# Performance work log

Measured on AMD Instinct MI355X. Metric: run time of the kernel, lower is better.

The kernel has to match this reference:

```python
import jax, jax.numpy as jnp
import numpy as np

N = 100000   # nodes
E = 800000   # edges
H = 64       # hidden_channels (also input feature dim via lazy Linear)
OUT = 2      # out_channels
G = 64       # graphs in batch
EPS = 1e-5   # BatchNorm eps
N_PRE, N_CONV, N_POST = 3, 6, 3


def setup_inputs() -> dict:
    key = jax.random.key(0)
    ks = jax.random.split(key, 20)
    s = 0.1
    inp = {
        "x": jax.random.normal(ks[0], (N, H), jnp.float32),
        "edge_index": jax.random.randint(ks[1], (2, E), 0, N, dtype=jnp.int64),
        "batch": jnp.sort(jax.random.randint(ks[2], (N,), 0, G, dtype=jnp.int64)),
        # pre-processing MLP + BN params
        "pre_W": jax.random.normal(ks[3], (N_PRE, H, H), jnp.float32) * s,
        "pre_b": jax.random.normal(ks[4], (N_PRE, H), jnp.float32) * s,
        "pre_g": jnp.ones((N_PRE, H), jnp.float32),
        "pre_beta": jnp.zeros((N_PRE, H), jnp.float32),
        # GCNConv params (weight + bias per layer)
        "conv_W": jax.random.normal(ks[5], (N_CONV, H, H), jnp.float32) * s,
        "conv_b": jax.random.normal(ks[6], (N_CONV, H), jnp.float32) * s,
        # post-processing MLP + BN params
        "post_W": jax.random.normal(ks[7], (N_POST, H, H), jnp.float32) * s,
        "post_b": jax.random.normal(ks[8], (N_POST, H), jnp.float32) * s,
        "post_g": jnp.ones((N_POST, H), jnp.float32),
        "post_beta": jnp.zeros((N_POST, H), jnp.float32),
        # final head: H->H, H->H, H->OUT
        "fin_W0": jax.random.normal(ks[9], (H, H), jnp.float32) * s,
        "fin_b0": jax.random.normal(ks[10], (H,), jnp.float32) * s,
        "fin_W1": jax.random.normal(ks[11], (H, H), jnp.float32) * s,
        "fin_b1": jax.random.normal(ks[12], (H,), jnp.float32) * s,
        "fin_W2": jax.random.normal(ks[13], (H, OUT), jnp.float32) * s,
        "fin_b2": jax.random.normal(ks[14], (OUT,), jnp.float32) * s,
    }
    return inp


def _bn(h, g, b):
    # BatchNorm1d, training mode: biased batch statistics over node dim
    m = h.mean(0)
    v = h.var(0)
    return (h - m) * jax.lax.rsqrt(v + EPS) * g + b


def _gcn(h, src, dst, dinv, W, b):
    # PyG GCNConv: h' = D^-1/2 (A+I) D^-1/2 (h W) + b, sum-aggregated at dst
    hw = h @ W                                   # [N,H]
    norm = dinv[src] * dinv[dst]                 # [E]
    agg = jax.ops.segment_sum(hw[src] * norm[:, None], dst, num_segments=N)
    agg = agg + hw * (dinv * dinv)[:, None]      # self-loop contribution
    return agg + b


def reference(x, edge_index, batch, pre_W, pre_b, pre_g, pre_beta,
              conv_W, conv_b, post_W, post_b, post_g, post_beta,
              fin_W0, fin_b0, fin_W1, fin_b1, fin_W2, fin_b2):
    src, dst = edge_index[0], edge_index[1]
    # gcn_norm degree with self-loops (in-degree at dst), edge_weight = 1
    deg = jax.ops.segment_sum(jnp.ones((E,), x.dtype), dst, num_segments=N) + 1.0
    dinv = jax.lax.rsqrt(deg)

    h = x
    # pre-processing: Linear -> BN, relu except last
    for i in range(N_PRE):
        h = _bn(h @ pre_W[i] + pre_b[i], pre_g[i], pre_beta[i])
        if i != N_PRE - 1:
            h = jax.nn.relu(h)
    # GCNConv stack with residual adds
    for i in range(N_CONV):
        h = _gcn(h, src, dst, dinv, conv_W[i], conv_b[i]) + h
        if i != N_CONV - 1:
            h = jax.nn.relu(h)
    # post-processing: Linear -> BN, relu except last
    for i in range(N_POST):
        h = _bn(h @ post_W[i] + post_b[i], post_g[i], post_beta[i])
        if i != N_POST - 1:
            h = jax.nn.relu(h)
    # global_mean_pool over graphs
    counts = jax.ops.segment_sum(jnp.ones((N,), h.dtype), batch, num_segments=G)
    pooled = jax.ops.segment_sum(h, batch, num_segments=G) / jnp.maximum(counts, 1.0)[:, None]
    # final head (dropout is identity in eval)
    z = jax.nn.relu(pooled @ fin_W0 + fin_b0)
    z = jax.nn.relu(z @ fin_W1 + fin_b1)
    return z @ fin_W2 + fin_b2
```

## Files before the change

### kernel.cpp

```cpp
#include <hip/hip_runtime.h>

#define N_NODES 100000
#define N_EDGES 800000
#define HID 64
#define NGRAPH 64
#define OUTC 2
#define BN_EPS 1e-5f
#define GEMM_BLK ((N_NODES + 63) / 64)
#define POOL_SUB 16
#define BSHIFT 11
#define NBUCK 64
#define NBUCK_ACT ((N_NODES + (1 << BSHIFT) - 1) >> BSHIFT)
#define NEB_BLK ((N_EDGES + 2047) / 2048)

typedef __attribute__((ext_vector_type(8))) short bf16x8;
typedef __attribute__((ext_vector_type(4))) float f32x4;
typedef __attribute__((ext_vector_type(2))) float f32x2;

__device__ __forceinline__ unsigned short f2bf(float f) {
    unsigned int u = __float_as_uint(f);
    u = (u + 0x7FFFu + ((u >> 16) & 1u)) >> 16;
    return (unsigned short)u;
}
__device__ __forceinline__ float bflo(unsigned int u) { return __uint_as_float(u << 16); }
__device__ __forceinline__ float bfhi(unsigned int u) { return __uint_as_float(u & 0xFFFF0000u); }
__device__ __forceinline__ unsigned int bfpack(float a, float b) {
    return (unsigned int)f2bf(a) | ((unsigned int)f2bf(b) << 16);
}
__device__ __forceinline__ f32x2 bfpair(unsigned int w) {
    f32x2 p;
    p.x = __uint_as_float(w << 16);
    p.y = __uint_as_float(w & 0xFFFF0000u);
    return p;
}
__device__ __forceinline__ f32x2 pk_add(f32x2 a, f32x2 b) {
    f32x2 d;
    asm("v_pk_add_f32 %0, %1, %2" : "=v"(d) : "v"(a), "v"(b));
    return d;
}

template <int IN_MODE, bool IN_FP32, bool ADD_BIAS, bool ROW_SCALE, bool STATS>
__global__ __launch_bounds__(256) void k_gemm(const void* __restrict__ Xv,
                                              const float* __restrict__ W,
                                              const float* __restrict__ bias,
                                              const float* __restrict__ dinv,
                                              const float* __restrict__ scsh,
                                              unsigned short* __restrict__ Y,
                                              float* __restrict__ partial, int n) {
    __shared__ __align__(16) unsigned short sXb[64][72];
    __shared__ __align__(16) unsigned short sWT[64][72];
    __shared__ float sDinv[64];
    const int tid  = threadIdx.x;
    const int row0 = blockIdx.x * 64;

    #pragma unroll
    for (int i = tid; i < 1024; i += 256) {
        int k = i >> 4, c4 = (i & 15) << 2;
        float4 w = *reinterpret_cast<const float4*>(&W[k * 64 + c4]);
        sWT[c4 + 0][k] = f2bf(w.x);
        sWT[c4 + 1][k] = f2bf(w.y);
        sWT[c4 + 2][k] = f2bf(w.z);
        sWT[c4 + 3][k] = f2bf(w.w);
    }
    if (IN_FP32) {
        const float* X = (const float*)Xv;
        #pragma unroll
        for (int f = tid; f < 1024; f += 256) {
            int r = f >> 4, c4 = (f & 15) << 2;
            float4 v = make_float4(0.f, 0.f, 0.f, 0.f);
            if (row0 + r < n)
                v = *reinterpret_cast<const float4*>(&X[(size_t)(row0 + r) * HID + c4]);
            if (IN_MODE >= 1) {
                float4 sc = *reinterpret_cast<const float4*>(&scsh[c4]);
                float4 sh = *reinterpret_cast<const float4*>(&scsh[64 + c4]);
                v.x = v.x * sc.x + sh.x; v.y = v.y * sc.y + sh.y;
                v.z = v.z * sc.z + sh.z; v.w = v.w * sc.w + sh.w;
                if (IN_MODE == 2) {
                    v.x = fmaxf(v.x, 0.f); v.y = fmaxf(v.y, 0.f);
                    v.z = fmaxf(v.z, 0.f); v.w = fmaxf(v.w, 0.f);
                }
            }
            sXb[r][c4 + 0] = f2bf(v.x);
            sXb[r][c4 + 1] = f2bf(v.y);
            sXb[r][c4 + 2] = f2bf(v.z);
            sXb[r][c4 + 3] = f2bf(v.w);
        }
    } else {
        const unsigned short* X = (const unsigned short*)Xv;
        #pragma unroll
        for (int f = tid; f < 512; f += 256) {
            int r = f >> 3, c8 = (f & 7) << 3;
            uint4 u = make_uint4(0u, 0u, 0u, 0u);
            if (row0 + r < n)
                u = *reinterpret_cast<const uint4*>(&X[(size_t)(row0 + r) * HID + c8]);
            if (IN_MODE >= 1) {
                float v[8];
                v[0] = bflo(u.x); v[1] = bfhi(u.x);
                v[2] = bflo(u.y); v[3] = bfhi(u.y);
                v[4] = bflo(u.z); v[5] = bfhi(u.z);
                v[6] = bflo(u.w); v[7] = bfhi(u.w);
                #pragma unroll
                for (int k = 0; k < 8; ++k) {
                    v[k] = v[k] * scsh[c8 + k] + scsh[64 + c8 + k];
                    if (IN_MODE == 2) v[k] = fmaxf(v[k], 0.f);
                }
                u.x = bfpack(v[0], v[1]); u.y = bfpack(v[2], v[3]);
                u.z = bfpack(v[4], v[5]); u.w = bfpack(v[6], v[7]);
            }
            *reinterpret_cast<uint4*>(&sXb[r][c8]) = u;
        }
    }
    if (ROW_SCALE && tid < 64)
        sDinv[tid] = (row0 + tid < n) ? dinv[row0 + tid] : 0.f;
    __syncthreads();

    const int lane = tid & 63;
    const int wv   = tid >> 6;
    const int cl   = lane & 15;
    const int kg   = lane >> 4;
    const int col  = (wv << 4) + cl;

    const f32x4 zero = {0.f, 0.f, 0.f, 0.f};
    f32x4 acc[4];
    #pragma unroll
    for (int m = 0; m < 4; ++m) acc[m] = zero;

    #pragma unroll
    for (int k0 = 0; k0 < 64; k0 += 32) {
        bf16x8 bfrag = *reinterpret_cast<const bf16x8*>(&sWT[col][k0 + (kg << 3)]);
        #pragma unroll
        for (int m = 0; m < 4; ++m) {
            bf16x8 afrag = *reinterpret_cast<const bf16x8*>(&sXb[(m << 4) + cl][k0 + (kg << 3)]);
            acc[m] = __builtin_amdgcn_mfma_f32_16x16x32_bf16(afrag, bfrag, acc[m], 0, 0, 0);
        }
    }

    const float bb = ADD_BIAS ? bias[col] : 0.f;
    float colS = 0.f, colQ = 0.f;
    #pragma unroll
    for (int m = 0; m < 4; ++m) {
        #pragma unroll
        for (int j = 0; j < 4; ++j) {
            int rl = (m << 4) + (kg << 2) + j;
            int r  = row0 + rl;
            if (r < n) {
                float s = ROW_SCALE ? sDinv[rl] : 1.f;
                float o = acc[m][j] * s + bb;
                Y[(size_t)r * HID + col] = f2bf(o);
                if (STATS) { colS += o; colQ += o * o; }
            }
        }
    }
    if (STATS) {
        colS += __shfl_xor(colS, 16); colQ += __shfl_xor(colQ, 16);
        colS += __shfl_xor(colS, 32); colQ += __shfl_xor(colQ, 32);
        if (kg == 0) {
            partial[blockIdx.x * 128 + col]      = colS;
            partial[blockIdx.x * 128 + 64 + col] = colQ;
        }
    }
}

__global__ __launch_bounds__(256) void k_statsfin(const float* __restrict__ partial,
                                                  const float* __restrict__ g,
                                                  const float* __restrict__ beta,
                                                  float* __restrict__ scsh, int n) {
    int c = blockIdx.x, t = threadIdx.x;
    float S = 0.f, Q = 0.f;
    for (int b = t; b < GEMM_BLK; b += 256) {
        S += partial[b * 128 + c];
        Q += partial[b * 128 + 64 + c];
    }
    __shared__ float ss[256], sq[256];
    ss[t] = S; sq[t] = Q;
    __syncthreads();
    for (int off = 128; off > 0; off >>= 1) {
        if (t < off) { ss[t] += ss[t + off]; sq[t] += sq[t + off]; }
        __syncthreads();
    }
    if (t == 0) {
        float nf = (float)n;
        float m  = ss[0] / nf;
        float v  = sq[0] / nf - m * m;
        float sc = rsqrtf(v + BN_EPS) * g[c];
        scsh[c]      = sc;
        scsh[64 + c] = beta[c] - m * sc;
    }
}

__global__ __launch_bounds__(256) void k_hist(const int* __restrict__ dst,
                                              int* __restrict__ histmat) {
    __shared__ int lh[NBUCK];
    int t = threadIdx.x;
    if (t < NBUCK) lh[t] = 0;
    __syncthreads();
    int base = blockIdx.x * 2048;
    for (int i = t; i < 2048; i += 256) {
        int e = base + i;
        if (e < N_EDGES) atomicAdd(&lh[dst[e] >> BSHIFT], 1);
    }
    __syncthreads();
    if (t < NBUCK) histmat[blockIdx.x * NBUCK + t] = lh[t];
}

__global__ __launch_bounds__(256) void k_escan(const int* __restrict__ histmat,
                                               int* __restrict__ blockoff,
                                               int* __restrict__ bucketbase) {
    __shared__ int csum[4][NBUCK];
    __shared__ int cbase[4][NBUCK];
    __shared__ int tot[NBUCK + 1];
    int t = threadIdx.x;
    int b = t & 63, c = t >> 6;
    const int CHUNK = (NEB_BLK + 3) / 4;
    int lo = c * CHUNK, hi = min(lo + CHUNK, NEB_BLK);
    int s = 0;
    #pragma unroll 8
    for (int blk = lo; blk < hi; ++blk) s += histmat[blk * NBUCK + b];
    csum[c][b] = s;
    __syncthreads();
    if (t < NBUCK) {
        int r = 0;
        #pragma unroll
        for (int c2 = 0; c2 < 4; ++c2) { cbase[c2][t] = r; r += csum[c2][t]; }
        tot[t] = r;
    }
    __syncthreads();
    if (t == 0) {
        int r = 0;
        for (int b2 = 0; b2 < NBUCK; ++b2) { int v = tot[b2]; tot[b2] = r; r += v; }
        tot[NBUCK] = r;
    }
    __syncthreads();
    if (t <= NBUCK) bucketbase[t] = tot[t];
    int r = cbase[c][b];
    #pragma unroll 8
    for (int blk = lo; blk < hi; ++blk) {
        blockoff[blk * NBUCK + b] = r;
        r += histmat[blk * NBUCK + b];
    }
}

__global__ __launch_bounds__(256) void k_reorder(const int* __restrict__ src,
                                                 const int* __restrict__ dst,
                                                 const int* __restrict__ blockoff,
                                                 const int* __restrict__ bucketbase,
                                                 int2* __restrict__ esort) {
    __shared__ int lcur[NBUCK];
    int t = threadIdx.x;
    if (t < NBUCK) lcur[t] = 0;
    __syncthreads();
    int base = blockIdx.x * 2048;
    for (int i = t; i < 2048; i += 256) {
        int e = base + i;
        if (e < N_EDGES) {
            int d = dst[e];
            int b = d >> BSHIFT;
            int r = atomicAdd(&lcur[b], 1);
            esort[bucketbase[b] + blockoff[blockIdx.x * NBUCK + b] + r] =
                make_int2(src[e], d);
        }
    }
}

__global__ __launch_bounds__(256) void k_csr(const int2* __restrict__ esort,
                                             const int* __restrict__ bucketbase,
                                             int* __restrict__ rowptr,
                                             int* __restrict__ colidx,
                                             float* __restrict__ dinv) {
    __shared__ int lh[1 << BSHIFT];
    __shared__ int ctot[256];
    int t = threadIdx.x;
    int b = blockIdx.x;
    int node0 = b << BSHIFT;
    int nNodes = min(1 << BSHIFT, N_NODES - node0);
    int e0 = bucketbase[b], e1 = bucketbase[b + 1];
    #pragma unroll
    for (int i = t; i < (1 << BSHIFT); i += 256) lh[i] = 0;
    __syncthreads();
    for (int e = e0 + t; e < e1; e += 256)
        atomicAdd(&lh[esort[e].y - node0], 1);
    __syncthreads();
    int c0 = t * 8;
    int cnt[8];
    int s = 0;
    #pragma unroll
    for (int j = 0; j < 8; ++j) { cnt[j] = lh[c0 + j]; s += cnt[j]; }
    ctot[t] = s;
    __syncthreads();
    int v = ctot[t];
    for (int off = 1; off < 256; off <<= 1) {
        int x = (t >= off) ? ctot[t - off] : 0;
        __syncthreads();
        ctot[t] += x;
        __syncthreads();
    }
    int run = ctot[t] - v;
    #pragma unroll
    for (int j = 0; j < 8; ++j) {
        int idx = c0 + j;
        int cv = cnt[j];
        lh[idx] = run;
        if (idx < nNodes) {
            rowptr[node0 + idx] = e0 + run;
            dinv[node0 + idx]   = rsqrtf((float)cv + 1.f);
        }
        run += cv;
    }
    __syncthreads();
    for (int e = e0 + t; e < e1; e += 256) {
        int2 ed = esort[e];
        int r = atomicAdd(&lh[ed.y - node0], 1);
        colidx[e0 + r] = ed.x;
    }
    if (b == 0 && t == 0) rowptr[N_NODES] = N_EDGES;
}

template <int IN_MODE, bool RELU>
__global__ __launch_bounds__(256) void k_gather(const int* __restrict__ rowptr,
                                                const int* __restrict__ colidx,
                                                const unsigned short* __restrict__ HWb,
                                                const unsigned short* __restrict__ Hin,
                                                const float* __restrict__ dinv,
                                                const float* __restrict__ bias,
                                                const float* __restrict__ scsh,
                                                unsigned short* __restrict__ Out) {
    __shared__ float red[4][8][64];
    const int wv   = threadIdx.x >> 6;
    const int d    = blockIdx.x * 4 + wv;
    const int lane = threadIdx.x & 63;
    const int slot = lane >> 3;
    const int c8   = (lane & 7) << 3;
    const int j0 = rowptr[d], j1 = rowptr[d + 1];

    f32x2 a0 = {0.f, 0.f}, a1 = {0.f, 0.f}, a2 = {0.f, 0.f}, a3 = {0.f, 0.f};

    if (slot == 7) {
        uint4 v = *reinterpret_cast<const uint4*>(&HWb[(size_t)d * HID + c8]);
        a0 = pk_add(a0, bfpair(v.x));
        a1 = pk_add(a1, bfpair(v.y));
        a2 = pk_add(a2, bfpair(v.z));
        a3 = pk_add(a3, bfpair(v.w));
    }
    for (int j = j0 + slot; j < j1; j += 8) {
        int s = colidx[j];
        uint4 v = *reinterpret_cast<const uint4*>(&HWb[(size_t)s * HID + c8]);
        a0 = pk_add(a0, bfpair(v.x));
        a1 = pk_add(a1, bfpair(v.y));
        a2 = pk_add(a2, bfpair(v.z));
        a3 = pk_add(a3, bfpair(v.w));
    }

    *reinterpret_cast<float4*>(&red[wv][slot][c8])     = make_float4(a0.x, a0.y, a1.x, a1.y);
    *reinterpret_cast<float4*>(&red[wv][slot][c8 + 4]) = make_float4(a2.x, a2.y, a3.x, a3.y);
    __syncthreads();

    const int col = lane;
    float s = 0.f;
    #pragma unroll
    for (int t2 = 0; t2 < 8; ++t2) s += red[wv][t2][col];

    float h = bflo((unsigned int)Hin[(size_t)d * HID + col]);
    if (IN_MODE == 1) h = h * scsh[col] + scsh[64 + col];
    float o = s * dinv[d] + bias[col] + h;
    if (RELU) o = fmaxf(o, 0.f);
    Out[(size_t)d * HID + col] = f2bf(o);
}

__device__ __forceinline__ int lowerb(const int* __restrict__ b, int n, int v) {
    int lo = 0, hi = n;
    while (lo < hi) { int m = (lo + hi) >> 1; if (b[m] < v) lo = m + 1; else hi = m; }
    return lo;
}

__global__ __launch_bounds__(256) void k_pool1(const unsigned short* __restrict__ Y,
                                               const int* __restrict__ batch,
                                               float* __restrict__ partial2) {
    int g  = blockIdx.x >> 4;
    int sb = blockIdx.x & 15;
    int tid = threadIdx.x, col = tid & 63, rg = tid >> 6;
    int lo = lowerb(batch, N_NODES, g);
    int hi = lowerb(batch, N_NODES, g + 1);
    int cnt = hi - lo;
    int st = lo + (int)(((long long)cnt * sb) >> 4);
    int en = lo + (int)(((long long)cnt * (sb + 1)) >> 4);
    float s = 0.f;
    for (int r = st + rg; r < en; r += 4)
        s += bflo((unsigned int)Y[(size_t)r * HID + col]);
    __shared__ float ls[4][64];
    ls[rg][col] = s;
    __syncthreads();
    if (tid < 64)
        partial2[(size_t)blockIdx.x * 64 + tid] =
            ls[0][tid] + ls[1][tid] + ls[2][tid] + ls[3][tid];
}

__global__ __launch_bounds__(256) void k_final(const float* __restrict__ partial2,
                                               const int* __restrict__ batch,
                                               const float* __restrict__ scsh,
                                               const float* __restrict__ W0,
                                               const float* __restrict__ b0,
                                               const float* __restrict__ W1,
                                               const float* __restrict__ b1,
                                               const float* __restrict__ W2,
                                               const float* __restrict__ b2,
                                               float* __restrict__ out) {
    __shared__ float sA[64][68];
    __shared__ float sC[64][68];
    __shared__ float sW[64][64];
    __shared__ int sOff[NGRAPH + 1];
    const int tid = threadIdx.x;
    const int tr = tid >> 4, tc = tid & 15;

    if (tid <= NGRAPH) sOff[tid] = lowerb(batch, N_NODES, tid);
    {
        const float4* w = reinterpret_cast<const float4*>(W0);
        float4* s = reinterpret_cast<float4*>(&sW[0][0]);
        #pragma unroll
        for (int i = tid; i < 1024; i += 256) s[i] = w[i];
    }
    __syncthreads();

    for (int i = tid; i < NGRAPH * HID; i += 256) {
        int g = i >> 6, c = i & 63;
        float S = 0.f;
        #pragma unroll
        for (int sb = 0; sb < POOL_SUB; ++sb)
            S += partial2[(size_t)(g * POOL_SUB + sb) * 64 + c];
        int cnt = sOff[g + 1] - sOff[g];
        float v = 0.f;
        if (cnt > 0) v = (S / (float)cnt) * scsh[c] + scsh[64 + c];
        sA[g][c] = v;
    }
    __syncthreads();

    {
        float4 acc[4];
        #pragma unroll
        for (int i = 0; i < 4; ++i) acc[i] = make_float4(0.f, 0.f, 0.f, 0.f);
        #pragma unroll 16
        for (int k = 0; k < 64; ++k) {
            const float4 bv = *reinterpret_cast<const float4*>(&sW[k][tc << 2]);
            float a[4];
            #pragma unroll
            for (int i = 0; i < 4; ++i) a[i] = sA[(tr << 2) + i][k];
            #pragma unroll
            for (int i = 0; i < 4; ++i) {
                acc[i].x += a[i] * bv.x; acc[i].y += a[i] * bv.y;
                acc[i].z += a[i] * bv.z; acc[i].w += a[i] * bv.w;
            }
        }
        float4 bb = *reinterpret_cast<const float4*>(&b0[tc << 2]);
        #pragma unroll
        for (int i = 0; i < 4; ++i) {
            float4 o;
            o.x = fmaxf(acc[i].x + bb.x, 0.f);
            o.y = fmaxf(acc[i].y + bb.y, 0.f);
            o.z = fmaxf(acc[i].z + bb.z, 0.f);
            o.w = fmaxf(acc[i].w + bb.w, 0.f);
            *reinterpret_cast<float4*>(&sC[(tr << 2) + i][tc << 2]) = o;
        }
    }
    __syncthreads();
    {
        const float4* w = reinterpret_cast<const float4*>(W1);
        float4* s = reinterpret_cast<float4*>(&sW[0][0]);
        #pragma unroll
        for (int i = tid; i < 1024; i += 256) s[i] = w[i];
    }
    __syncthreads();

    {
        float4 acc[4];
        #pragma unroll
        for (int i = 0; i < 4; ++i) acc[i] = make_float4(0.f, 0.f, 0.f, 0.f);
        #pragma unroll 16
        for (int k = 0; k < 64; ++k) {
            const float4 bv = *reinterpret_cast<const float4*>(&sW[k][tc << 2]);
            float a[4];
            #pragma unroll
            for (int i = 0; i < 4; ++i) a[i] = sC[(tr << 2) + i][k];
            #pragma unroll
            for (int i = 0; i < 4; ++i) {
                acc[i].x += a[i] * bv.x; acc[i].y += a[i] * bv.y;
                acc[i].z += a[i] * bv.z; acc[i].w += a[i] * bv.w;
            }
        }
        float4 bb = *reinterpret_cast<const float4*>(&b1[tc << 2]);
        #pragma unroll
        for (int i = 0; i < 4; ++i) {
            float4 o;
            o.x = fmaxf(acc[i].x + bb.x, 0.f);
            o.y = fmaxf(acc[i].y + bb.y, 0.f);
            o.z = fmaxf(acc[i].z + bb.z, 0.f);
            o.w = fmaxf(acc[i].w + bb.w, 0.f);
            *reinterpret_cast<float4*>(&sA[(tr << 2) + i][tc << 2]) = o;
        }
    }
    __syncthreads();

    if (tid < NGRAPH * OUTC) {
        int r = tid >> 1, c = tid & 1;
        float acc = b2[c];
        #pragma unroll 8
        for (int k = 0; k < 64; ++k) acc += sA[r][k] * W2[k * OUTC + c];
        out[tid] = acc;
    }
}

extern "C" void kernel_launch(void* const* d_in, const int* in_sizes, int n_in,
                              void* d_out, int out_size, void* d_ws, size_t ws_size,
                              hipStream_t stream) {
    const float* x        = (const float*)d_in[0];
    const int*   ei       = (const int*)d_in[1];
    const int*   batch    = (const int*)d_in[2];
    const float* pre_W    = (const float*)d_in[3];
    const float* pre_b    = (const float*)d_in[4];
    const float* pre_g    = (const float*)d_in[5];
    const float* pre_beta = (const float*)d_in[6];
    const float* conv_W   = (const float*)d_in[7];
    const float* conv_b   = (const float*)d_in[8];
    const float* post_W   = (const float*)d_in[9];
    const float* post_b   = (const float*)d_in[10];
    const float* post_g   = (const float*)d_in[11];
    const float* post_beta= (const float*)d_in[12];
    const float* fW0 = (const float*)d_in[13];
    const float* fb0 = (const float*)d_in[14];
    const float* fW1 = (const float*)d_in[15];
    const float* fb1 = (const float*)d_in[16];
    const float* fW2 = (const float*)d_in[17];
    const float* fb2 = (const float*)d_in[18];
    float* out = (float*)d_out;

    const size_t NH = (size_t)N_NODES * HID;
    unsigned short* Ab = (unsigned short*)d_ws;
    unsigned short* Bb = Ab + NH;
    unsigned short* Cb = Bb + NH;
    float* dinv     = (float*)(Cb + NH);
    float* partial  = dinv + N_NODES;
    float* scsh     = partial + (size_t)GEMM_BLK*128;
    float* partial2 = scsh + 6 * 128;
    int* histmat    = (int*)(partial2 + NGRAPH * POOL_SUB * 64);
    int* blockoff   = histmat + NEB_BLK * NBUCK;
    int* bucketbase = blockoff + NEB_BLK * NBUCK;
    int* rowptr     = bucketbase + NBUCK + 1;
    int* colidx     = rowptr + N_NODES + 1;
    size_t eoff = (size_t)(colidx + N_EDGES - (int*)d_ws);
    eoff = (eoff + 1) & ~(size_t)1;
    int2* esort     = (int2*)((int*)d_ws + eoff);

    const int* srcp = ei;
    const int* dstp = ei + N_EDGES;
    const int gNode4 = (N_NODES + 3) / 4;

    k_hist<<<NEB_BLK, 256, 0, stream>>>(dstp, histmat);
    k_escan<<<1, 256, 0, stream>>>(histmat, blockoff, bucketbase);
    k_reorder<<<NEB_BLK, 256, 0, stream>>>(srcp, dstp, blockoff, bucketbase, esort);
    k_csr<<<NBUCK_ACT, 256, 0, stream>>>(esort, bucketbase, rowptr, colidx, dinv);

    k_gemm<0, true,  true, false, true><<<GEMM_BLK, 256, 0, stream>>>(x, pre_W, pre_b, nullptr, nullptr, Ab, partial, N_NODES);
    k_statsfin<<<64, 256, 0, stream>>>(partial, pre_g, pre_beta, scsh + 0 * 128, N_NODES);

    k_gemm<2, false, true, false, true><<<GEMM_BLK, 256, 0, stream>>>(Ab, pre_W + 4096, pre_b + 64, nullptr, scsh + 0 * 128, Cb, partial, N_NODES);
    k_statsfin<<<64, 256, 0, stream>>>(partial, pre_g + 64, pre_beta + 64, scsh + 1 * 128, N_NODES);

    k_gemm<2, false, true, false, true><<<GEMM_BLK, 256, 0, stream>>>(Cb, pre_W + 2 * 4096, pre_b + 128, nullptr, scsh + 1 * 128, Ab, partial, N_NODES);
    k_statsfin<<<64, 256, 0, stream>>>(partial, pre_g + 128, pre_beta + 128, scsh + 2 * 128, N_NODES);

    for (int i = 0; i < 6; ++i) {
        const unsigned short* in = (i & 1) ? Cb : Ab;
        unsigned short*     outb = (i & 1) ? Ab : Cb;
        const float* Wl = conv_W + i * 4096;
        const float* bl = conv_b + i * 64;
        if (i == 0)
            k_gemm<1, false, false, true, false><<<GEMM_BLK, 256, 0, stream>>>(in, Wl, nullptr, dinv, scsh + 2 * 128, Bb, nullptr, N_NODES);
        else
            k_gemm<0, false, false, true, false><<<GEMM_BLK, 256, 0, stream>>>(in, Wl, nullptr, dinv, nullptr, Bb, nullptr, N_NODES);

        if (i == 0)
            k_gather<1, true ><<<gNode4, 256, 0, stream>>>(rowptr, colidx, Bb, in, dinv, bl, scsh + 2 * 128, outb);
        else if (i != 5)
            k_gather<0, true ><<<gNode4, 256, 0, stream>>>(rowptr, colidx, Bb, in, dinv, bl, nullptr, outb);
        else
            k_gather<0, false><<<gNode4, 256, 0, stream>>>(rowptr, colidx, Bb, in, dinv, bl, nullptr, outb);
    }

    k_gemm<0, false, true, false, true><<<GEMM_BLK, 256, 0, stream>>>(Ab, post_W, post_b, nullptr, nullptr, Cb, partial, N_NODES);
    k_statsfin<<<64, 256, 0, stream>>>(partial, post_g, post_beta, scsh + 3 * 128, N_NODES);

    k_gemm<2, false, true, false, true><<<GEMM_BLK, 256, 0, stream>>>(Cb, post_W + 4096, post_b + 64, nullptr, scsh + 3 * 128, Ab, partial, N_NODES);
    k_statsfin<<<64, 256, 0, stream>>>(partial, post_g + 64, post_beta + 64, scsh + 4 * 128, N_NODES);

    k_gemm<2, false, true, false, true><<<GEMM_BLK, 256, 0, stream>>>(Ab, post_W + 2 * 4096, post_b + 128, nullptr, scsh + 4 * 128, Cb, partial, N_NODES);
    k_statsfin<<<64, 256, 0, stream>>>(partial, post_g + 128, post_beta + 128, scsh + 5 * 128, N_NODES);

    k_pool1<<<NGRAPH * POOL_SUB, 256, 0, stream>>>(Cb, batch, partial2);
    k_final<<<1, 256, 0, stream>>>(partial2, batch, scsh + 5 * 128,
                                   fW0, fb0, fW1, fb1, fW2, fb2, out);
}
```

Before: 479.5 us.

## Fuse GCN aggregation and weight GEMM into one kernel using aggregate-then-transform

Replaces the per-layer GEMM plus gather pair with a single k_conv kernel. Using linearity, it first aggregates dinv-prescaled features, then multiplies the 64-node tile by W with bf16 MFMA in shared memory. Activations are kept stored pre-scaled by dinv, and a new rdinv array recovers the residual term. This removes one full N×64 write/read round trip and one launch per layer. In exchange it adds bf16 rounding of the scaled features, 1024-thread blocks with heavy LDS use that may cut occupancy for the gather, and an extra k_mkg pass before the first layer.

```diff
diff --git a/kernel.cpp b/kernel.cpp
--- a/kernel.cpp
+++ b/kernel.cpp
@@ -266,7 +266,8 @@
                                              const int* __restrict__ bucketbase,
                                              int* __restrict__ rowptr,
                                              int* __restrict__ colidx,
-                                             float* __restrict__ dinv) {
+                                             float* __restrict__ dinv,
+                                             float* __restrict__ rdinv) {
     __shared__ int lh[1 << BSHIFT];
     __shared__ int ctot[256];
     int t = threadIdx.x;
@@ -302,7 +303,9 @@
         lh[idx] = run;
         if (idx < nNodes) {
             rowptr[node0 + idx] = e0 + run;
-            dinv[node0 + idx]   = rsqrtf((float)cv + 1.f);
+            float dg = (float)cv + 1.f;
+            dinv[node0 + idx]  = rsqrtf(dg);
+            rdinv[node0 + idx] = sqrtf(dg);
         }
         run += cv;
     }
@@ -315,55 +318,135 @@
     if (b == 0 && t == 0) rowptr[N_NODES] = N_EDGES;
 }
 
-template <int IN_MODE, bool RELU>
-__global__ __launch_bounds__(256) void k_gather(const int* __restrict__ rowptr,
-                                                const int* __restrict__ colidx,
-                                                const unsigned short* __restrict__ HWb,
-                                                const unsigned short* __restrict__ Hin,
-                                                const float* __restrict__ dinv,
-                                                const float* __restrict__ bias,
-                                                const float* __restrict__ scsh,
-                                                unsigned short* __restrict__ Out) {
-    __shared__ float red[4][8][64];
-    const int wv   = threadIdx.x >> 6;
-    const int d    = blockIdx.x * 4 + wv;
-    const int lane = threadIdx.x & 63;
+__global__ __launch_bounds__(256) void k_mkg(const unsigned short* __restrict__ H,
+                                             const float* __restrict__ scsh,
+                                             const float* __restrict__ dinv,
+                                             unsigned short* __restrict__ G) {
+    int i = blockIdx.x * 256 + threadIdx.x;
+    if (i >= N_NODES * 8) return;
+    int row = i >> 3, c8 = (i & 7) << 3;
+    uint4 u = *reinterpret_cast<const uint4*>(&H[(size_t)row * HID + c8]);
+    float di = dinv[row];
+    float v[8];
+    v[0] = bflo(u.x); v[1] = bfhi(u.x);
+    v[2] = bflo(u.y); v[3] = bfhi(u.y);
+    v[4] = bflo(u.z); v[5] = bfhi(u.z);
+    v[6] = bflo(u.w); v[7] = bfhi(u.w);
+    #pragma unroll
+    for (int k = 0; k < 8; ++k)
+        v[k] = (v[k] * scsh[c8 + k] + scsh[64 + c8 + k]) * di;
+    uint4 o;
+    o.x = bfpack(v[0], v[1]); o.y = bfpack(v[2], v[3]);
+    o.z = bfpack(v[4], v[5]); o.w = bfpack(v[6], v[7]);
+    *reinterpret_cast<uint4*>(&G[(size_t)row * HID + c8]) = o;
+}
+
+template <bool LAST>
+__global__ __launch_bounds__(1024) void k_conv(const int* __restrict__ rowptr,
+                                               const int* __restrict__ colidx,
+                                               const unsigned short* __restrict__ G,
+                                               const float* __restrict__ dinv,
+                                               const float* __restrict__ rdinv,
+                                               const float* __restrict__ W,
+                                               const float* __restrict__ bias,
+                                               unsigned short* __restrict__ OutT) {
+    __shared__ __align__(16) unsigned short sXb[64][72];
+    __shared__ __align__(16) unsigned short sG[64][72];
+    __shared__ __align__(16) unsigned short sWT[64][72];
+    __shared__ float red[16][8][64];
+    __shared__ float sDinv[64], sRD[64];
+    const int tid   = threadIdx.x;
+    const int node0 = blockIdx.x * 64;
+
+    {
+        int k = tid >> 4, c4 = (tid & 15) << 2;
+        float4 w = *reinterpret_cast<const float4*>(&W[k * 64 + c4]);
+        sWT[c4 + 0][k] = f2bf(w.x);
+        sWT[c4 + 1][k] = f2bf(w.y);
+        sWT[c4 + 2][k] = f2bf(w.z);
+        sWT[c4 + 3][k] = f2bf(w.w);
+    }
+    if (tid < 64) {
+        int nd = node0 + tid;
+        sDinv[tid] = (nd < N_NODES) ? dinv[nd] : 0.f;
+        sRD[tid]   = (nd < N_NODES) ? rdinv[nd] : 0.f;
+    }
+
+    const int wv   = tid >> 6;
+    const int lane = tid & 63;
     const int slot = lane >> 3;
     const int c8   = (lane & 7) << 3;
-    const int j0 = rowptr[d], j1 = rowptr[d + 1];
-
-    f32x2 a0 = {0.f, 0.f}, a1 = {0.f, 0.f}, a2 = {0.f, 0.f}, a3 = {0.f, 0.f};
-
-    if (slot == 7) {
-        uint4 v = *reinterpret_cast<const uint4*>(&HWb[(size_t)d * HID + c8]);
-        a0 = pk_add(a0, bfpair(v.x));
-        a1 = pk_add(a1, bfpair(v.y));
-        a2 = pk_add(a2, bfpair(v.z));
-        a3 = pk_add(a3, bfpair(v.w));
-    }
-    for (int j = j0 + slot; j < j1; j += 8) {
-        int s = colidx[j];
-        uint4 v = *reinterpret_cast<const uint4*>(&HWb[(size_t)s * HID + c8]);
-        a0 = pk_add(a0, bfpair(v.x));
-        a1 = pk_add(a1, bfpair(v.y));
-        a2 = pk_add(a2, bfpair(v.z));
-        a3 = pk_add(a3, bfpair(v.w));
-    }
-
-    *reinterpret_cast<float4*>(&red[wv][slot][c8])     = make_float4(a0.x, a0.y, a1.x, a1.y);
-    *reinterpret_cast<float4*>(&red[wv][slot][c8 + 4]) = make_float4(a2.x, a2.y, a3.x, a3.y);
-    __syncthreads();
-
-    const int col = lane;
-    float s = 0.f;
-    #pragma unroll
-    for (int t2 = 0; t2 < 8; ++t2) s += red[wv][t2][col];
-
-    float h = bflo((unsigned int)Hin[(size_t)d * HID + col]);
-    if (IN_MODE == 1) h = h * scsh[col] + scsh[64 + col];
-    float o = s * dinv[d] + bias[col] + h;
-    if (RELU) o = fmaxf(o, 0.f);
-    Out[(size_t)d * HID + col] = f2bf(o);
+
+    #pragma unroll 1
+    for (int it = 0; it < 4; ++it) {
+        const int dl = (wv << 2) + it;
+        const int d  = node0 + dl;
+        const bool valid = d < N_NODES;
+
+        f32x2 a0 = {0.f, 0.f}, a1 = {0.f, 0.f}, a2 = {0.f, 0.f}, a3 = {0.f, 0.f};
+        if (valid) {
+            if (slot == 7) {
+                uint4 v = *reinterpret_cast<const uint4*>(&G[(size_t)d * HID + c8]);
+                a0 = pk_add(a0, bfpair(v.x));
+                a1 = pk_add(a1, bfpair(v.y));
+                a2 = pk_add(a2, bfpair(v.z));
+                a3 = pk_add(a3, bfpair(v.w));
+            }
+            const int j0 = rowptr[d], j1 = rowptr[d + 1];
+            for (int j = j0 + slot; j < j1; j += 8) {
+                int s = colidx[j];
+                uint4 v = *reinterpret_cast<const uint4*>(&G[(size_t)s * HID + c8]);
+                a0 = pk_add(a0, bfpair(v.x));
+                a1 = pk_add(a1, bfpair(v.y));
+                a2 = pk_add(a2, bfpair(v.z));
+                a3 = pk_add(a3, bfpair(v.w));
+            }
+        }
+        *reinterpret_cast<float4*>(&red[wv][slot][c8])     = make_float4(a0.x, a0.y, a1.x, a1.y);
+        *reinterpret_cast<float4*>(&red[wv][slot][c8 + 4]) = make_float4(a2.x, a2.y, a3.x, a3.y);
+        __builtin_amdgcn_wave_barrier();
+        float s = 0.f;
+        #pragma unroll
+        for (int t2 = 0; t2 < 8; ++t2) s += red[wv][t2][lane];
+
+        if (valid) {
+            float z = s * sDinv[dl];
+            sXb[dl][lane] = f2bf(z);
+            sG[dl][lane]  = G[(size_t)d * HID + lane];
+        } else {
+            sXb[dl][lane] = 0;
+            sG[dl][lane]  = 0;
+        }
+    }
+    __syncthreads();
+
+    const int rt = wv & 3, ct = wv >> 2;
+    const int cl = lane & 15, kg = lane >> 4;
+    const int col = (ct << 4) + cl;
+
+    f32x4 acc = {0.f, 0.f, 0.f, 0.f};
+    #pragma unroll
+    for (int k0 = 0; k0 < 64; k0 += 32) {
+        bf16x8 bfrag = *reinterpret_cast<const bf16x8*>(&sWT[col][k0 + (kg << 3)]);
+        bf16x8 afrag = *reinterpret_cast<const bf16x8*>(&sXb[(rt << 4) + cl][k0 + (kg << 3)]);
+        acc = __builtin_amdgcn_mfma_f32_16x16x32_bf16(afrag, bfrag, acc, 0, 0, 0);
+    }
+
+    const float bb = bias[col];
+    #pragma unroll
+    for (int j = 0; j < 4; ++j) {
+        int rl = (rt << 4) + (kg << 2) + j;
+        int r  = node0 + rl;
+        if (r < N_NODES) {
+            float h = bflo((unsigned int)sG[rl][col]) * sRD[rl];
+            float o = acc[j] + bb + h;
+            if (!LAST) {
+                o = fmaxf(o, 0.f);
+                o *= sDinv[rl];
+            }
+            OutT[(size_t)r * HID + col] = f2bf(o);
+        }
+    }
 }
 
 __device__ __forceinline__ int lowerb(const int* __restrict__ b, int n, int v) {
@@ -468,7 +551,6 @@
         for (int i = tid; i < 1024; i += 256) s[i] = w[i];
     }
     __syncthreads();
-
     {
         float4 acc[4];
         #pragma unroll
@@ -536,7 +618,8 @@
     unsigned short* Bb = Ab + NH;
     unsigned short* Cb = Bb + NH;
     float* dinv     = (float*)(Cb + NH);
-    float* partial  = dinv + N_NODES;
+    float* rdinv    = dinv + N_NODES;
+    float* partial  = rdinv + N_NODES;
     float* scsh     = partial + (size_t)GEMM_BLK*128;
     float* partial2 = scsh + 6 * 128;
     int* histmat    = (int*)(partial2 + NGRAPH * POOL_SUB * 64);
@@ -550,12 +633,11 @@
 
     const int* srcp = ei;
     const int* dstp = ei + N_EDGES;
-    const int gNode4 = (N_NODES + 3) / 4;
 
     k_hist<<<NEB_BLK, 256, 0, stream>>>(dstp, histmat);
     k_escan<<<1, 256, 0, stream>>>(histmat, blockoff, bucketbase);
     k_reorder<<<NEB_BLK, 256, 0, stream>>>(srcp, dstp, blockoff, bucketbase, esort);
-    k_csr<<<NBUCK_ACT, 256, 0, stream>>>(esort, bucketbase, rowptr, colidx, dinv);
+    k_csr<<<NBUCK_ACT, 256, 0, stream>>>(esort, bucketbase, rowptr, colidx, dinv, rdinv);
 
     k_gemm<0, true,  true, false, true><<<GEMM_BLK, 256, 0, stream>>>(x, pre_W, pre_b, nullptr, nullptr, Ab, partial, N_NODES);
     k_statsfin<<<64, 256, 0, stream>>>(partial, pre_g, pre_beta, scsh + 0 * 128, N_NODES);
@@ -566,23 +648,14 @@
     k_gemm<2, false, true, false, true><<<GEMM_BLK, 256, 0, stream>>>(Cb, pre_W + 2 * 4096, pre_b + 128, nullptr, scsh + 1 * 128, Ab, partial, N_NODES);
     k_statsfin<<<64, 256, 0, stream>>>(partial, pre_g + 128, pre_beta + 128, scsh + 2 * 128, N_NODES);
 
-    for (int i = 0; i < 6; ++i) {
-        const unsigned short* in = (i & 1) ? Cb : Ab;
-        unsigned short*     outb = (i & 1) ? Ab : Cb;
-        const float* Wl = conv_W + i * 4096;
-        const float* bl = conv_b + i * 64;
-        if (i == 0)
-            k_gemm<1, false, false, true, false><<<GEMM_BLK, 256, 0, stream>>>(in, Wl, nullptr, dinv, scsh + 2 * 128, Bb, nullptr, N_NODES);
-        else
-            k_gemm<0, false, false, true, false><<<GEMM_BLK, 256, 0, stream>>>(in, Wl, nullptr, dinv, nullptr, Bb, nullptr, N_NODES);
-
-        if (i == 0)
-            k_gather<1, true ><<<gNode4, 256, 0, stream>>>(rowptr, colidx, Bb, in, dinv, bl, scsh + 2 * 128, outb);
-        else if (i != 5)
-            k_gather<0, true ><<<gNode4, 256, 0, stream>>>(rowptr, colidx, Bb, in, dinv, bl, nullptr, outb);
-        else
-            k_gather<0, false><<<gNode4, 256, 0, stream>>>(rowptr, colidx, Bb, in, dinv, bl, nullptr, outb);
-    }
+    k_mkg<<<(N_NODES * 8 + 255) / 256, 256, 0, stream>>>(Ab, scsh + 2 * 128, dinv, Bb);
+
+    k_conv<false><<<GEMM_BLK, 1024, 0, stream>>>(rowptr, colidx, Bb, dinv, rdinv, conv_W + 0 * 4096, conv_b + 0 * 64, Cb);
+    k_conv<false><<<GEMM_BLK, 1024, 0, stream>>>(rowptr, colidx, Cb, dinv, rdinv, conv_W + 1 * 4096, conv_b + 1 * 64, Bb);
+    k_conv<false><<<GEMM_BLK, 1024, 0, stream>>>(rowptr, colidx, Bb, dinv, rdinv, conv_W + 2 * 4096, conv_b + 2 * 64, Cb);
+    k_conv<false><<<GEMM_BLK, 1024, 0, stream>>>(rowptr, colidx, Cb, dinv, rdinv, conv_W + 3 * 4096, conv_b + 3 * 64, Bb);
+    k_conv<false><<<GEMM_BLK, 1024, 0, stream>>>(rowptr, colidx, Bb, dinv, rdinv, conv_W + 4 * 4096, conv_b + 4 * 64, Cb);
+    k_conv<true ><<<GEMM_BLK, 1024, 0, stream>>>(rowptr, colidx, Cb, dinv, rdinv, conv_W + 5 * 4096, conv_b + 5 * 64, Ab);
 
     k_gemm<0, false, true, false, true><<<GEMM_BLK, 256, 0, stream>>>(Ab, post_W, post_b, nullptr, nullptr, Cb, partial, N_NODES);
     k_statsfin<<<64, 256, 0, stream>>>(partial, post_g, post_beta, scsh + 3 * 128, N_NODES);
```

Measured after the change: 480.1 us. Within noise of the previous version (+0.1%).
